# Kernel tuning notes

Measured on AMD Instinct MI355X. Metric: run time of the kernel, lower is better.

Reference implementation:

```python
import jax, jax.numpy as jnp
import numpy as np
import math

B, S, DIM = 2, 2048, 1024
N_HEADS, N_KV = 16, 4
HD = DIM // N_HEADS          # 64
N_REP = N_HEADS // N_KV      # 4
ROPE_THETA = 5000.0


def _rope_tables(seqlen, head_dim, theta):
    freqs = 1.0 / (theta ** (np.arange(0, head_dim, 2, dtype=np.float32) / head_dim))
    angles = np.outer(np.arange(seqlen, dtype=np.float32), freqs)  # [S, HD/2]
    return jnp.asarray(np.cos(angles)), jnp.asarray(np.sin(angles))


def setup_inputs() -> dict:
    key = jax.random.key(0)
    ks = jax.random.split(key, 6)
    x = jax.random.normal(ks[0], (B, S, DIM), dtype=jnp.float32)
    cos, sin = _rope_tables(S, HD, ROPE_THETA)
    # additive causal mask: 0 on/below diagonal, -inf above
    mask = jnp.where(jnp.tril(jnp.ones((S, S), dtype=bool)), 0.0, -jnp.inf).astype(jnp.float32)
    wq = jax.random.normal(ks[1], (DIM, N_HEADS * HD), dtype=jnp.float32) * 0.02
    wk = jax.random.normal(ks[2], (DIM, N_KV * HD), dtype=jnp.float32) * 0.02
    wv = jax.random.normal(ks[3], (DIM, N_KV * HD), dtype=jnp.float32) * 0.02
    wo = jax.random.normal(ks[4], (N_HEADS * HD, DIM), dtype=jnp.float32) * 0.02
    return {"x": x, "cos": cos, "sin": sin, "mask": mask,
            "wq": wq, "wk": wk, "wv": wv, "wo": wo}


def _apply_rope(t, cos, sin):
    # t: [B, S, H, HD]; even/odd interleaved pairs form complex numbers
    te, to = t[..., 0::2], t[..., 1::2]               # [B,S,H,HD/2]
    c = cos[None, :, None, :]
    s = sin[None, :, None, :]
    re = te * c - to * s
    im = te * s + to * c
    return jnp.stack([re, im], axis=-1).reshape(t.shape)  # re-interleave


def reference(x, cos, sin, mask, wq, wk, wv, wo):
    bsz, seqlen, _ = x.shape
    q = (x @ wq).reshape(bsz, seqlen, N_HEADS, HD)
    k = (x @ wk).reshape(bsz, seqlen, N_KV, HD)
    v = (x @ wv).reshape(bsz, seqlen, N_KV, HD)
    q = _apply_rope(q, cos, sin)
    k = _apply_rope(k, cos, sin)
    # GQA: group query heads as [kv_head g, rep r] instead of repeating K/V
    qg = q.reshape(bsz, seqlen, N_KV, N_REP, HD)
    scores = jnp.einsum('bsgrd,btgd->bgrst', qg, k) / math.sqrt(HD)  # [B,G,R,S,S]
    scores = scores + mask[None, None, None, :, :]
    p = jax.nn.softmax(scores, axis=-1)
    out = jnp.einsum('bgrst,btgd->bsgrd', p, v)       # [B,S,G,R,HD]
    out = out.reshape(bsz, seqlen, N_HEADS * HD)
    return out @ wo
```

## Files before the change

### kernel.cpp

```cpp
#include <hip/hip_runtime.h>
#include <math.h>

#define S_LEN 2048
#define B_SZ 2

typedef __bf16 bf16_8 __attribute__((ext_vector_type(8)));
typedef float  f32_4  __attribute__((ext_vector_type(4)));

__device__ __forceinline__ unsigned short ftob(float f) {
  union { __bf16 h; unsigned short u; } cv;
  cv.h = (__bf16)f;
  return cv.u;
}

__device__ __forceinline__ void gll16(const unsigned short* g, unsigned short* l) {
  __builtin_amdgcn_global_load_lds(
      (const __attribute__((address_space(1))) unsigned int*)g,
      (__attribute__((address_space(3))) unsigned int*)l, 16, 0, 0);
}

#define QSCALE (0.125f * 1.44269504f)


__device__ __forceinline__ void tr_tile(const float* __restrict__ W,
                                        unsigned short* __restrict__ Wt,
                                        int N, int bx, int by, float (*T)[33])
{
  const int k0 = by * 32, n0 = bx * 32;
  const int r = threadIdx.x >> 3, c4 = (threadIdx.x & 7) * 4;
  const float4 v = *(const float4*)&W[(size_t)(k0 + r) * N + n0 + c4];
  T[r][c4 + 0] = v.x; T[r][c4 + 1] = v.y;
  T[r][c4 + 2] = v.z; T[r][c4 + 3] = v.w;
  __syncthreads();
  ushort4 o;
  o.x = ftob(T[c4 + 0][r]); o.y = ftob(T[c4 + 1][r]);
  o.z = ftob(T[c4 + 2][r]); o.w = ftob(T[c4 + 3][r]);
  *(ushort4*)&Wt[(size_t)(n0 + r) * 1024 + k0 + c4] = o;
}

__global__ __launch_bounds__(256) void prep(
    const float* __restrict__ x, const float* __restrict__ wq,
    const float* __restrict__ wk, const float* __restrict__ wv,
    const float* __restrict__ wo,
    unsigned short* __restrict__ xb, unsigned short* __restrict__ wqkvt,
    unsigned short* __restrict__ wot)
{
  __shared__ float T[32][33];
  const int idx = blockIdx.x;
  if (idx < 1024) {
    tr_tile(wq, wqkvt, 1024, idx & 31, idx >> 5, T);
  } else if (idx < 1280) {
    const int i = idx - 1024;
    tr_tile(wk, wqkvt + 1024 * 1024, 256, i & 7, i >> 3, T);
  } else if (idx < 1536) {
    const int i = idx - 1280;
    tr_tile(wv, wqkvt + 1280 * 1024, 256, i & 7, i >> 3, T);
  } else if (idx < 2560) {
    const int i = idx - 1536;
    tr_tile(wo, wot, 1024, i & 31, i >> 5, T);
  } else {
    const int i = idx - 2560;
#pragma unroll
    for (int j = 0; j < 4; ++j) {
      const int id = i * 1024 + (int)threadIdx.x + j * 256;
      const float4 v = ((const float4*)x)[id];
      ushort4 o;
      o.x = ftob(v.x); o.y = ftob(v.y); o.z = ftob(v.z); o.w = ftob(v.w);
      ((ushort4*)xb)[id] = o;
    }
  }
}

#define G64DB_STAGE(A_, B_, bo_, k0_)                                           \
  do {                                                                          \
    const int r = tid >> 2, o8 = (tid & 3) * 8;                                 \
    gll16(&A_[(size_t)(bm + r) * 1024 + (k0_) + o8], &sm[(bo_) + tid * 8]);     \
    gll16(&A_[(size_t)(bm + r) * 1024 + (k0_) + 32 + o8],                       \
          &sm[(bo_) + 2048 + tid * 8]);                                         \
    gll16(&B_[(size_t)(bn0 * 128 + r) * 1024 + (k0_) + o8],                     \
          &sm[(bo_) + 4096 + tid * 8]);                                         \
    gll16(&B_[(size_t)(bn0 * 128 + r + 64) * 1024 + (k0_) + o8],                \
          &sm[(bo_) + 6144 + tid * 8]);                                         \
    gll16(&B_[(size_t)(bn0 * 128 + r) * 1024 + (k0_) + 32 + o8],                \
          &sm[(bo_) + 8192 + tid * 8]);                                         \
    gll16(&B_[(size_t)(bn0 * 128 + r + 64) * 1024 + (k0_) + 32 + o8],           \
          &sm[(bo_) + 10240 + tid * 8]);                                        \
  } while (0)

#define G64DB_KLOOP(A_, B_)                                                     \
  G64DB_STAGE(A_, B_, 0, 0);                                                    \
  __syncthreads();                                                              \
  for (int s = 0; s < 16; ++s) {                                                \
    const int bo = (s & 1) * 12288;                                             \
    if (s < 15) G64DB_STAGE(A_, B_, bo ^ 12288, (s + 1) * 64);                  \
    bf16_8 af[2][2], bf[2][4];                                                  \
    _Pragma("unroll")                                                           \
    for (int ks = 0; ks < 2; ++ks) {                                            \
      _Pragma("unroll")                                                         \
      for (int mt = 0; mt < 2; ++mt)                                            \
        af[ks][mt] = *(const bf16_8*)&sm[bo + ks * 2048 +                       \
                                         (mh + mt * 16 + l16) * 32 + quad * 8]; \
      _Pragma("unroll")                                                         \
      for (int nt = 0; nt < 4; ++nt)                                            \
        bf[ks][nt] = *(const bf16_8*)&sm[bo + 4096 + ks * 4096 +                \
                                         (nh + nt * 16 + l16) * 32 + quad * 8]; \
    }                                                                           \
    _Pragma("unroll")                                                           \
    for (int ks = 0; ks < 2; ++ks)                                              \
      _Pragma("unroll")                                                         \
      for (int mt = 0; mt < 2; ++mt)                                            \
        _Pragma("unroll")                                                       \
        for (int nt = 0; nt < 4; ++nt)                                          \
          acc[mt][nt] = __builtin_amdgcn_mfma_f32_16x16x32_bf16(                \
              af[ks][mt], bf[ks][nt], acc[mt][nt], 0, 0, 0);                    \
    __syncthreads();                                                            \
  }

__global__ __launch_bounds__(256, 3) void gemm_qkv(
    const unsigned short* __restrict__ A, const unsigned short* __restrict__ Bt,
    unsigned short* __restrict__ qb, unsigned short* __restrict__ Kimg,
    unsigned short* __restrict__ Vimg,
    const float* __restrict__ cosT, const float* __restrict__ sinT)
{
  __shared__ unsigned short sm[24576];
  const int bm = blockIdx.y * 64, bn0 = blockIdx.x;
  const int tid = threadIdx.x;
  const int w = tid >> 6, lane = tid & 63, l16 = lane & 15, quad = lane >> 4;
  const int mh = (w & 1) * 32, nh = (w >> 1) * 64;

  f32_4 acc[2][4];
#pragma unroll
  for (int mt = 0; mt < 2; ++mt)
#pragma unroll
    for (int nt = 0; nt < 4; ++nt) acc[mt][nt] = (f32_4){0.f, 0.f, 0.f, 0.f};

  G64DB_KLOOP(A, Bt);

  const int colbase = bn0 * 128;
  if (colbase < 1024) {
#pragma unroll
    for (int mt = 0; mt < 2; ++mt)
#pragma unroll
      for (int r = 0; r < 4; ++r) {
        const int row = bm + mh + mt * 16 + quad * 4 + r;
        const int s = row & (S_LEN - 1);
#pragma unroll
        for (int nt = 0; nt < 4; ++nt) {
          const int col = colbase + nh + nt * 16 + l16;
          float val = acc[mt][nt][r];
          const float pv = __shfl_xor(val, 1);
          const int fi = (col & 63) >> 1;
          const float cc = cosT[s * 32 + fi], ss = sinT[s * 32 + fi];
          val = (l16 & 1) ? fmaf(pv, ss, val * cc) : fmaf(val, cc, -(pv * ss));
          qb[(size_t)row * 1024 + col] = ftob(val * QSCALE);
        }
      }
  } else if (colbase < 1280) {
#pragma unroll
    for (int mt = 0; mt < 2; ++mt)
#pragma unroll
      for (int r = 0; r < 4; ++r) {
        const int row = bm + mh + mt * 16 + quad * 4 + r;
        const int s = row & (S_LEN - 1), bi = row >> 11;
        const int tile = s >> 6, key = s & 63;
#pragma unroll
        for (int nt = 0; nt < 4; ++nt) {
          const int col = colbase + nh + nt * 16 + l16;
          float val = acc[mt][nt][r];
          const float pv = __shfl_xor(val, 1);
          const int fi = (col & 63) >> 1;
          const float cc = cosT[s * 32 + fi], ss = sinT[s * 32 + fi];
          val = (l16 & 1) ? fmaf(pv, ss, val * cc) : fmaf(val, cc, -(pv * ss));
          const int gcol = col - 1024, g = gcol >> 6, d = gcol & 63;
          Kimg[(size_t)((bi * 4 + g) * 32 + tile) * 4096 + key * 64 +
               (((d >> 3) ^ (key & 7)) * 8) + (d & 7)] = ftob(val);
        }
      }
  } else {
    const int bi = bm >> 11, t0 = (bm & 2047) >> 6;
    const int gp = (bn0 - 10) * 2;
    __syncthreads();
    {
      unsigned short* Ts = sm + (w >> 1) * 4608;
#pragma unroll
      for (int mt = 0; mt < 2; ++mt)
#pragma unroll
        for (int nt = 0; nt < 4; ++nt) {
          const int keyb = mh + mt * 16 + quad * 4;
          const int d = nt * 16 + l16;
          ushort4 pk;
#pragma unroll
          for (int r = 0; r < 4; ++r) ((unsigned short*)&pk)[r] = ftob(acc[mt][nt][r]);
          *(ushort4*)&Ts[d * 72 + keyb] = pk;
        }
    }
    __syncthreads();
#pragma unroll
    for (int it = 0; it < 4; ++it) {
      const int c = tid + it * 256;
      const int img = c >> 9, cc = c & 511;
      const int d = cc >> 3, ch = cc & 7;
      const uint4 v = *(const uint4*)&sm[img * 4608 + d * 72 + ch * 8];
      *(uint4*)&Vimg[(size_t)((bi * 4 + gp + img) * 32 + t0) * 4096 + d * 64 +
                     ((ch ^ (d & 7)) * 8)] = v;
    }
  }
}

__global__ __launch_bounds__(256, 2) void gemm_wo(
    const unsigned short* __restrict__ A, const unsigned short* __restrict__ Bt,
    float* __restrict__ C)
{
  __shared__ unsigned short sm[24576];
  const int bm = blockIdx.y * 64, bn0 = blockIdx.x;
  const int tid = threadIdx.x;
  const int w = tid >> 6, lane = tid & 63, l16 = lane & 15, quad = lane >> 4;
  const int mh = (w & 1) * 32, nh = (w >> 1) * 64;

  f32_4 acc[2][4];
#pragma unroll
  for (int mt = 0; mt < 2; ++mt)
#pragma unroll
    for (int nt = 0; nt < 4; ++nt) acc[mt][nt] = (f32_4){0.f, 0.f, 0.f, 0.f};

  G64DB_KLOOP(A, Bt);

#pragma unroll
  for (int mt = 0; mt < 2; ++mt)
#pragma unroll
    for (int r = 0; r < 4; ++r) {
      const int row = bm + mh + mt * 16 + quad * 4 + r;
#pragma unroll
      for (int nt = 0; nt < 4; ++nt)
        C[(size_t)row * 1024 + bn0 * 128 + nh + nt * 16 + l16] = acc[mt][nt][r];
    }
}

__global__ __launch_bounds__(512, 4) void flash_attn_v10(
    const unsigned short* __restrict__ Q, const unsigned short* __restrict__ Kimg,
    const unsigned short* __restrict__ Vimg, unsigned short* __restrict__ O)
{
  __shared__ unsigned short Ks[8192];
  __shared__ unsigned short Vs[8192];
  __shared__ unsigned short Ps[8][2048];
  __shared__ float lbuf[4][2][64];
  const int id = blockIdx.x;
  const int gb = id & 7;
  const int g = gb & 3, b = gb >> 2;
  const int j = id >> 3;
  const int qc = (j < 32) ? (63 - j) : (j - 32);
  const int tid = threadIdx.x;
  const int w = tid >> 6, lane = tid & 63, l16 = lane & 15, quad = lane >> 4;
  const int hw = w & 3, par = w >> 2;
  const int h = g * 4 + hw;
  const int qbase = qc * 32;
  const int swz = l16 & 7;
  unsigned short* ps = Ps[w];

  bf16_8 bq[2][2];
#pragma unroll
  for (int qf = 0; qf < 2; ++qf) {
    const unsigned short* qp =
        Q + ((size_t)(b * S_LEN + qbase + qf * 16 + l16)) * 1024 + h * 64;
    bq[qf][0] = *(const bf16_8*)(qp + quad * 8);
    bq[qf][1] = *(const bf16_8*)(qp + 32 + quad * 8);
  }

  f32_4 acc[2][4];
#pragma unroll
  for (int qf = 0; qf < 2; ++qf)
#pragma unroll
    for (int mt = 0; mt < 4; ++mt) acc[qf][mt] = (f32_4){0.f, 0.f, 0.f, 0.f};
  float l_part[2] = {0.f, 0.f};

  const unsigned short* kim = Kimg + (size_t)(gb * 32) * 4096;
  const unsigned short* vim = Vimg + (size_t)(gb * 32) * 4096;
  const int ntiles = (qc >> 1) + 1;
  const int steps = (ntiles + 1) >> 1;

  for (int s = 0; s < steps; ++s) {
    __syncthreads();
    {
      const unsigned short* kp = kim + (size_t)s * 8192;
      const unsigned short* vp = vim + (size_t)s * 8192;
      gll16(kp + tid * 8, &Ks[tid * 8]);
      gll16(kp + (tid + 512) * 8, &Ks[(tid + 512) * 8]);
      gll16(vp + tid * 8, &Vs[tid * 8]);
      gll16(vp + (tid + 512) * 8, &Vs[(tid + 512) * 8]);
    }
    __syncthreads();

    const int tile = 2 * s + par;
    if (tile < ntiles) {
      const bool diag = (tile == ntiles - 1);
      const unsigned short* ks = Ks + par * 4096;
      const unsigned short* vs = Vs + par * 4096;
#pragma unroll
      for (int mt = 0; mt < 4; ++mt) {
        const int krow = (mt * 16 + l16) * 64;
        const bf16_8 kf0 = *(const bf16_8*)&ks[krow + (quad ^ swz) * 8];
        const bf16_8 kf1 = *(const bf16_8*)&ks[krow + ((4 + quad) ^ swz) * 8];
#pragma unroll
        for (int qf = 0; qf < 2; ++qf) {
          f32_4 z = (f32_4){0.f, 0.f, 0.f, 0.f};
          __builtin_amdgcn_s_setprio(1);
          z = __builtin_amdgcn_mfma_f32_16x16x32_bf16(kf0, bq[qf][0], z, 0, 0, 0);
          z = __builtin_amdgcn_mfma_f32_16x16x32_bf16(kf1, bq[qf][1], z, 0, 0, 0);
          __builtin_amdgcn_s_setprio(0);
          ushort4 pk;
#pragma unroll
          for (int r = 0; r < 4; ++r) {
            float pv = __builtin_amdgcn_exp2f(z[r]);
            if (diag) {
              const int keyl = mt * 16 + quad * 4 + r;
              const int ql = (qc & 1) * 32 + qf * 16 + l16;
              pv = (keyl > ql) ? 0.f : pv;
            }
            l_part[qf] += pv;
            ((unsigned short*)&pk)[r] = ftob(pv);
          }
          *(ushort4*)&ps[(qf * 16 + l16) * 64 +
                         (((2 * mt + (quad >> 1)) ^ swz) * 8) + (quad & 1) * 4] = pk;
        }
      }
      bf16_8 pf[2][2];
#pragma unroll
      for (int qf = 0; qf < 2; ++qf) {
        const int prow = (qf * 16 + l16) * 64;
        pf[qf][0] = *(const bf16_8*)&ps[prow + ((quad ^ swz) * 8)];
        pf[qf][1] = *(const bf16_8*)&ps[prow + (((4 + quad) ^ swz) * 8)];
      }
      __builtin_amdgcn_s_setprio(1);
#pragma unroll
      for (int mt = 0; mt < 4; ++mt) {
        const int vrow = (mt * 16 + l16) * 64;
        const bf16_8 vf0 = *(const bf16_8*)&vs[vrow + (quad ^ swz) * 8];
        const bf16_8 vf1 = *(const bf16_8*)&vs[vrow + ((4 + quad) ^ swz) * 8];
#pragma unroll
        for (int qf = 0; qf < 2; ++qf) {
          acc[qf][mt] = __builtin_amdgcn_mfma_f32_16x16x32_bf16(vf0, pf[qf][0], acc[qf][mt], 0, 0, 0);
          acc[qf][mt] = __builtin_amdgcn_mfma_f32_16x16x32_bf16(vf1, pf[qf][1], acc[qf][mt], 0, 0, 0);
        }
      }
      __builtin_amdgcn_s_setprio(0);
    }
  }

  __syncthreads();
  float* cb = (float*)&Ps[0][0];
  if (par == 1) {
    float* dst = cb + hw * 2048;
#pragma unroll
    for (int qf = 0; qf < 2; ++qf)
#pragma unroll
      for (int mt = 0; mt < 4; ++mt)
#pragma unroll
        for (int r = 0; r < 4; ++r)
          dst[(qf * 16 + mt * 4 + r) * 64 + lane] = acc[qf][mt][r];
    lbuf[hw][0][lane] = l_part[0];
    lbuf[hw][1][lane] = l_part[1];
  }
  __syncthreads();
  if (par == 0) {
    const float* src = cb + hw * 2048;
#pragma unroll
    for (int qf = 0; qf < 2; ++qf)
#pragma unroll
      for (int mt = 0; mt < 4; ++mt)
#pragma unroll
        for (int r = 0; r < 4; ++r)
          acc[qf][mt][r] += src[(qf * 16 + mt * 4 + r) * 64 + lane];
    l_part[0] += lbuf[hw][0][lane];
    l_part[1] += lbuf[hw][1][lane];

#pragma unroll
    for (int qf = 0; qf < 2; ++qf) {
      float l = l_part[qf];
      l += __shfl_xor(l, 16);
      l += __shfl_xor(l, 32);
      const float inv = 1.f / l;
      unsigned short* op =
          O + ((size_t)(b * S_LEN + qbase + qf * 16 + l16)) * 1024 + h * 64;
#pragma unroll
      for (int mt = 0; mt < 4; ++mt) {
        ushort4 ov;
#pragma unroll
        for (int r = 0; r < 4; ++r) ((unsigned short*)&ov)[r] = ftob(acc[qf][mt][r] * inv);
        *(ushort4*)&op[mt * 16 + quad * 4] = ov;
      }
    }
  }
}

extern "C" void kernel_launch(void* const* d_in, const int* in_sizes, int n_in,
                              void* d_out, int out_size, void* d_ws, size_t ws_size,
                              hipStream_t stream)
{
  const float* x    = (const float*)d_in[0];
  const float* cosT = (const float*)d_in[1];
  const float* sinT = (const float*)d_in[2];
  const float* wq   = (const float*)d_in[4];
  const float* wk   = (const float*)d_in[5];
  const float* wv   = (const float*)d_in[6];
  const float* wo   = (const float*)d_in[7];
  float* out = (float*)d_out;

  char* ws = (char*)d_ws;
  const size_t MB = 1024 * 1024;
  unsigned short* xb    = (unsigned short*)(ws);
  unsigned short* qb    = (unsigned short*)(ws + 8 * MB);
  unsigned short* wqkvt = (unsigned short*)(ws + 16 * MB);
  unsigned short* Kimg  = (unsigned short*)(ws + 19 * MB);
  unsigned short* Vimg  = (unsigned short*)(ws + 21 * MB);
  unsigned short* wot   = (unsigned short*)(ws + 23 * MB);

  prep<<<3584, 256, 0, stream>>>(x, wq, wk, wv, wo, xb, wqkvt, wot);
  gemm_qkv<<<dim3(12, 64), 256, 0, stream>>>(xb, wqkvt, qb, Kimg, Vimg, cosT, sinT);
  flash_attn_v10<<<512, 512, 0, stream>>>(qb, Kimg, Vimg, qb);
  gemm_wo<<<dim3(8, 64), 256, 0, stream>>>(qb, wot, out);
}
```

Measured before the change: 164.0 us.

## Keep P in registers via permuted K layout, double-buffer K/V, MFMA row sums

```diff
diff --git a/kernel.cpp b/kernel.cpp
--- a/kernel.cpp
+++ b/kernel.cpp
@@ -163,6 +163,8 @@
         const int row = bm + mh + mt * 16 + quad * 4 + r;
         const int s = row & (S_LEN - 1), bi = row >> 11;
         const int tile = s >> 6, key = s & 63;
+        const int kk = key & 31, jj = kk & 7;
+        const int rowp = ((key >> 5) << 5) + ((jj >> 2) << 4) + ((kk >> 3) << 2) + (jj & 3);
 #pragma unroll
         for (int nt = 0; nt < 4; ++nt) {
           const int col = colbase + nh + nt * 16 + l16;
@@ -172,8 +174,8 @@
           const float cc = cosT[s * 32 + fi], ss = sinT[s * 32 + fi];
           val = (l16 & 1) ? fmaf(pv, ss, val * cc) : fmaf(val, cc, -(pv * ss));
           const int gcol = col - 1024, g = gcol >> 6, d = gcol & 63;
-          Kimg[(size_t)((bi * 4 + g) * 32 + tile) * 4096 + key * 64 +
-               (((d >> 3) ^ (key & 7)) * 8) + (d & 7)] = ftob(val);
+          Kimg[(size_t)((bi * 4 + g) * 32 + tile) * 4096 + rowp * 64 +
+               (((d >> 3) ^ (rowp & 7)) * 8) + (d & 7)] = ftob(val);
         }
       }
   } else {
@@ -236,13 +238,12 @@
     }
 }
 
-__global__ __launch_bounds__(512, 4) void flash_attn_v10(
+__global__ __launch_bounds__(512, 4) void flash_attn_v11(
     const unsigned short* __restrict__ Q, const unsigned short* __restrict__ Kimg,
     const unsigned short* __restrict__ Vimg, unsigned short* __restrict__ O)
 {
-  __shared__ unsigned short Ks[8192];
-  __shared__ unsigned short Vs[8192];
-  __shared__ unsigned short Ps[8][2048];
+  __shared__ unsigned short Ks[2][8192];
+  __shared__ unsigned short Vs[2][8192];
   __shared__ float lbuf[4][2][64];
   const int id = blockIdx.x;
   const int gb = id & 7;
@@ -255,7 +256,10 @@
   const int h = g * 4 + hw;
   const int qbase = qc * 32;
   const int swz = l16 & 7;
-  unsigned short* ps = Ps[w];
+
+  union { bf16_8 v; unsigned short u[8]; } ones;
+#pragma unroll
+  for (int i = 0; i < 8; ++i) ones.u[i] = 0x3f80;
 
   bf16_8 bq[2][2];
 #pragma unroll
@@ -266,35 +270,44 @@
     bq[qf][1] = *(const bf16_8*)(qp + 32 + quad * 8);
   }
 
-  f32_4 acc[2][4];
-#pragma unroll
-  for (int qf = 0; qf < 2; ++qf)
+  f32_4 acc[2][4], acc_l[2];
+#pragma unroll
+  for (int qf = 0; qf < 2; ++qf) {
+    acc_l[qf] = (f32_4){0.f, 0.f, 0.f, 0.f};
 #pragma unroll
     for (int mt = 0; mt < 4; ++mt) acc[qf][mt] = (f32_4){0.f, 0.f, 0.f, 0.f};
-  float l_part[2] = {0.f, 0.f};
+  }
 
   const unsigned short* kim = Kimg + (size_t)(gb * 32) * 4096;
   const unsigned short* vim = Vimg + (size_t)(gb * 32) * 4096;
   const int ntiles = (qc >> 1) + 1;
   const int steps = (ntiles + 1) >> 1;
-
+  const int hq = (qc & 1) * 32;
+
+  {
+    gll16(kim + tid * 8, &Ks[0][tid * 8]);
+    gll16(kim + (tid + 512) * 8, &Ks[0][(tid + 512) * 8]);
+    gll16(vim + tid * 8, &Vs[0][tid * 8]);
+    gll16(vim + (tid + 512) * 8, &Vs[0][(tid + 512) * 8]);
+  }
   for (int s = 0; s < steps; ++s) {
+    const int c = s & 1;
     __syncthreads();
-    {
-      const unsigned short* kp = kim + (size_t)s * 8192;
-      const unsigned short* vp = vim + (size_t)s * 8192;
-      gll16(kp + tid * 8, &Ks[tid * 8]);
-      gll16(kp + (tid + 512) * 8, &Ks[(tid + 512) * 8]);
-      gll16(vp + tid * 8, &Vs[tid * 8]);
-      gll16(vp + (tid + 512) * 8, &Vs[(tid + 512) * 8]);
-    }
-    __syncthreads();
+    if (s + 1 < steps) {
+      const unsigned short* kp = kim + (size_t)(s + 1) * 8192;
+      const unsigned short* vp = vim + (size_t)(s + 1) * 8192;
+      gll16(kp + tid * 8, &Ks[c ^ 1][tid * 8]);
+      gll16(kp + (tid + 512) * 8, &Ks[c ^ 1][(tid + 512) * 8]);
+      gll16(vp + tid * 8, &Vs[c ^ 1][tid * 8]);
+      gll16(vp + (tid + 512) * 8, &Vs[c ^ 1][(tid + 512) * 8]);
+    }
 
     const int tile = 2 * s + par;
     if (tile < ntiles) {
       const bool diag = (tile == ntiles - 1);
-      const unsigned short* ks = Ks + par * 4096;
-      const unsigned short* vs = Vs + par * 4096;
+      const unsigned short* ks = &Ks[c][par * 4096];
+      const unsigned short* vs = &Vs[c][par * 4096];
+      union { bf16_8 v; unsigned int wd[4]; } pf[2][2];
 #pragma unroll
       for (int mt = 0; mt < 4; ++mt) {
         const int krow = (mt * 16 + l16) * 64;
@@ -307,28 +320,27 @@
           z = __builtin_amdgcn_mfma_f32_16x16x32_bf16(kf0, bq[qf][0], z, 0, 0, 0);
           z = __builtin_amdgcn_mfma_f32_16x16x32_bf16(kf1, bq[qf][1], z, 0, 0, 0);
           __builtin_amdgcn_s_setprio(0);
-          ushort4 pk;
+          float pv[4];
 #pragma unroll
           for (int r = 0; r < 4; ++r) {
-            float pv = __builtin_amdgcn_exp2f(z[r]);
+            float p = __builtin_amdgcn_exp2f(z[r]);
             if (diag) {
-              const int keyl = mt * 16 + quad * 4 + r;
-              const int ql = (qc & 1) * 32 + qf * 16 + l16;
-              pv = (keyl > ql) ? 0.f : pv;
+              const int keyl = ((mt >> 1) << 5) + quad * 8 + ((mt & 1) << 2) + r;
+              const int ql = hq + qf * 16 + l16;
+              p = (keyl > ql) ? 0.f : p;
             }
-            l_part[qf] += pv;
-            ((unsigned short*)&pk)[r] = ftob(pv);
+            pv[r] = p;
           }
-          *(ushort4*)&ps[(qf * 16 + l16) * 64 +
-                         (((2 * mt + (quad >> 1)) ^ swz) * 8) + (quad & 1) * 4] = pk;
+          pf[qf][mt >> 1].wd[(mt & 1) * 2 + 0] =
+              (unsigned int)ftob(pv[0]) | ((unsigned int)ftob(pv[1]) << 16);
+          pf[qf][mt >> 1].wd[(mt & 1) * 2 + 1] =
+              (unsigned int)ftob(pv[2]) | ((unsigned int)ftob(pv[3]) << 16);
         }
       }
-      bf16_8 pf[2][2];
 #pragma unroll
       for (int qf = 0; qf < 2; ++qf) {
-        const int prow = (qf * 16 + l16) * 64;
-        pf[qf][0] = *(const bf16_8*)&ps[prow + ((quad ^ swz) * 8)];
-        pf[qf][1] = *(const bf16_8*)&ps[prow + (((4 + quad) ^ swz) * 8)];
+        acc_l[qf] = __builtin_amdgcn_mfma_f32_16x16x32_bf16(ones.v, pf[qf][0].v, acc_l[qf], 0, 0, 0);
+        acc_l[qf] = __builtin_amdgcn_mfma_f32_16x16x32_bf16(ones.v, pf[qf][1].v, acc_l[qf], 0, 0, 0);
       }
       __builtin_amdgcn_s_setprio(1);
 #pragma unroll
@@ -338,8 +350,8 @@
         const bf16_8 vf1 = *(const bf16_8*)&vs[vrow + ((4 + quad) ^ swz) * 8];
 #pragma unroll
         for (int qf = 0; qf < 2; ++qf) {
-          acc[qf][mt] = __builtin_amdgcn_mfma_f32_16x16x32_bf16(vf0, pf[qf][0], acc[qf][mt], 0, 0, 0);
-          acc[qf][mt] = __builtin_amdgcn_mfma_f32_16x16x32_bf16(vf1, pf[qf][1], acc[qf][mt], 0, 0, 0);
+          acc[qf][mt] = __builtin_amdgcn_mfma_f32_16x16x32_bf16(vf0, pf[qf][0].v, acc[qf][mt], 0, 0, 0);
+          acc[qf][mt] = __builtin_amdgcn_mfma_f32_16x16x32_bf16(vf1, pf[qf][1].v, acc[qf][mt], 0, 0, 0);
         }
       }
       __builtin_amdgcn_s_setprio(0);
@@ -347,7 +359,7 @@
   }
 
   __syncthreads();
-  float* cb = (float*)&Ps[0][0];
+  float* cb = (float*)&Ks[0][0];
   if (par == 1) {
     float* dst = cb + hw * 2048;
 #pragma unroll
@@ -357,8 +369,8 @@
 #pragma unroll
         for (int r = 0; r < 4; ++r)
           dst[(qf * 16 + mt * 4 + r) * 64 + lane] = acc[qf][mt][r];
-    lbuf[hw][0][lane] = l_part[0];
-    lbuf[hw][1][lane] = l_part[1];
+    lbuf[hw][0][lane] = acc_l[0][0];
+    lbuf[hw][1][lane] = acc_l[1][0];
   }
   __syncthreads();
   if (par == 0) {
@@ -370,14 +382,10 @@
 #pragma unroll
         for (int r = 0; r < 4; ++r)
           acc[qf][mt][r] += src[(qf * 16 + mt * 4 + r) * 64 + lane];
-    l_part[0] += lbuf[hw][0][lane];
-    l_part[1] += lbuf[hw][1][lane];
 
 #pragma unroll
     for (int qf = 0; qf < 2; ++qf) {
-      float l = l_part[qf];
-      l += __shfl_xor(l, 16);
-      l += __shfl_xor(l, 32);
+      const float l = acc_l[qf][0] + lbuf[hw][qf][lane];
       const float inv = 1.f / l;
       unsigned short* op =
           O + ((size_t)(b * S_LEN + qbase + qf * 16 + l16)) * 1024 + h * 64;
@@ -416,6 +424,6 @@
 
   prep<<<3584, 256, 0, stream>>>(x, wq, wk, wv, wo, xb, wqkvt, wot);
   gemm_qkv<<<dim3(12, 64), 256, 0, stream>>>(xb, wqkvt, qb, Kimg, Vimg, cosT, sinT);
-  flash_attn_v10<<<512, 512, 0, stream>>>(qb, Kimg, Vimg, qb);
+  flash_attn_v11<<<512, 512, 0, stream>>>(qb, Kimg, Vimg, qb);
   gemm_wo<<<dim3(8, 64), 256, 0, stream>>>(qb, wot, out);
 }
```

Result: no change. 167.0 us (+1.9%).
